# Kernel tuning notes

Measured on AMD Instinct MI355X. Metric: run time of the kernel, lower is better.

## Reference

```python
import jax, jax.numpy as jnp
import numpy as np

IOU_THRESHOLD = 0.5

def cxcywh_to_xyxy(b):
    cx, cy, w, h = jnp.split(b, 4, axis=-1)
    return jnp.concatenate([cx - 0.5 * w, cy - 0.5 * h, cx + 0.5 * w, cy + 0.5 * h], axis=-1)

def batched_giou(p_xyxy, t_xyxy):
    # p_xyxy: [B, N, 4], t_xyxy: [B, T, 4] -> giou: [B, N, T]
    p = p_xyxy[:, :, None, :]  # [B, N, 1, 4]
    t = t_xyxy[:, None, :, :]  # [B, 1, T, 4]
    area_p = (p_xyxy[..., 2] - p_xyxy[..., 0]) * (p_xyxy[..., 3] - p_xyxy[..., 1])  # [B, N]
    area_t = (t_xyxy[..., 2] - t_xyxy[..., 0]) * (t_xyxy[..., 3] - t_xyxy[..., 1])  # [B, T]
    lt = jnp.maximum(p[..., :2], t[..., :2])
    rb = jnp.minimum(p[..., 2:], t[..., 2:])
    wh = jnp.clip(rb - lt, 0.0)
    inter = wh[..., 0] * wh[..., 1]  # [B, N, T]
    union = area_p[:, :, None] + area_t[:, None, :] - inter
    iou = inter / union
    # enclosing box
    lt_e = jnp.minimum(p[..., :2], t[..., :2])
    rb_e = jnp.maximum(p[..., 2:], t[..., 2:])
    wh_e = jnp.clip(rb_e - lt_e, 0.0)
    area_e = wh_e[..., 0] * wh_e[..., 1]
    return iou - (area_e - union) / area_e

def setup_inputs() -> dict:
    key = jax.random.key(0)
    k1, k2 = jax.random.split(key)
    B, N, T = 128, 900, 300
    pred_boxes = jax.random.uniform(k1, (B, N, 4), dtype=jnp.float32)
    target_boxes = jax.random.uniform(k2, (B, T, 4), dtype=jnp.float32)
    target_mask = jnp.ones((B, T), dtype=bool)
    return {"pred_boxes": pred_boxes, "target_boxes": target_boxes, "target_mask": target_mask}

def reference(pred_boxes, target_boxes, target_mask):
    # pred_boxes: [B, N, 4] cxcywh; target_boxes: [B, T, 4] cxcywh (padded)
    p_xyxy = cxcywh_to_xyxy(pred_boxes)
    t_xyxy = cxcywh_to_xyxy(target_boxes)
    giou = batched_giou(p_xyxy, t_xyxy)  # [B, N, T]
    max_iou = jnp.max(giou, axis=1)      # [B, T] best GIoU per target
    pred_idx = jnp.argmax(giou, axis=1)  # [B, T] matched query per target
    valid = target_mask & (max_iou >= IOU_THRESHOLD)  # [B, T] match kept
    return pred_idx, valid, max_iou
```

## Files before the change

kernel.cpp:

```cpp
#include <hip/hip_runtime.h>


#define BB 128
#define NN 900
#define TT 300
#define NSPLIT 9
#define NPB 100
#define NPW 25
#define TPL 5
#define ALANES 60
#define MARGIN 2e-5f

__device__ __forceinline__ float giou_exact(float4 pb, float4 tb) {
#pragma clang fp contract(off)
    float px0 = pb.x - 0.5f * pb.z, py0 = pb.y - 0.5f * pb.w;
    float px1 = pb.x + 0.5f * pb.z, py1 = pb.y + 0.5f * pb.w;
    float tx0 = tb.x - 0.5f * tb.z, ty0 = tb.y - 0.5f * tb.w;
    float tx1 = tb.x + 0.5f * tb.z, ty1 = tb.y + 0.5f * tb.w;
    float pa = (px1 - px0) * (py1 - py0);
    float ta = (tx1 - tx0) * (ty1 - ty0);
    float w  = fmaxf(fminf(px1, tx1) - fmaxf(px0, tx0), 0.f);
    float h  = fmaxf(fminf(py1, ty1) - fmaxf(py0, ty0), 0.f);
    float inter = w * h;
    float uni   = pa + ta - inter;
    float iou   = inter / uni;
    float ew = fmaxf(fmaxf(px1, tx1) - fminf(px0, tx0), 0.f);
    float eh = fmaxf(fmaxf(py1, ty1) - fminf(py0, ty0), 0.f);
    float ea = ew * eh;
    return iou - (ea - uni) / ea;
}

__global__ __launch_bounds__(256, 6) void matcher_scan_kernel(
    const float* __restrict__ pred,
    const float* __restrict__ tgt,
    float* __restrict__ pbest,
    float* __restrict__ psec,
    int*   __restrict__ pidx)
{
    __shared__ float4 sp[NPB];
    __shared__ float  spa[NPB];
    __shared__ float  sbv[4 * TT], ssv[4 * TT];
    __shared__ int    siv[4 * TT];

    const int ns  = blockIdx.x % NSPLIT;
    const int b   = blockIdx.x / NSPLIT;
    const int tid = threadIdx.x;
    const int l   = tid & 63;
    const int ng  = tid >> 6;

    if (tid < NPB) {
        const float4 pb = ((const float4*)pred)[b * NN + ns * NPB + tid];
        float4 q;
        q.x = pb.x - 0.5f * pb.z;
        q.y = pb.y - 0.5f * pb.w;
        q.z = pb.x + 0.5f * pb.z;
        q.w = pb.y + 0.5f * pb.w;
        sp[tid]  = q;
        spa[tid] = (q.z - q.x) * (q.w - q.y);
    }

    float tx0[TPL], ty0[TPL], tx1[TPL], ty1[TPL], ta[TPL];
    #pragma unroll
    for (int j = 0; j < TPL; ++j) {
        tx0[j] = ty0[j] = tx1[j] = ty1[j] = ta[j] = 0.f;
        if (l < ALANES) {
            const float4 tb = ((const float4*)tgt)[b * TT + j * ALANES + l];
            tx0[j] = tb.x - 0.5f * tb.z;
            ty0[j] = tb.y - 0.5f * tb.w;
            tx1[j] = tb.x + 0.5f * tb.z;
            ty1[j] = tb.y + 0.5f * tb.w;
            ta[j]  = (tx1[j] - tx0[j]) * (ty1[j] - ty0[j]);
        }
    }
    __syncthreads();

    float best[TPL], sec[TPL];
    int   bl[TPL];
    #pragma unroll
    for (int j = 0; j < TPL; ++j) { best[j] = -INFINITY; sec[j] = -INFINITY; bl[j] = 0; }

    const int k0 = ng * NPW;
    for (int k = 0; k < NPW; ++k) {
        const float4 p = sp[k0 + k];
        const float pa = spa[k0 + k];
        #pragma unroll
        for (int j = 0; j < TPL; ++j) {
            const float w   = fmaxf(fminf(p.z, tx1[j]) - fmaxf(p.x, tx0[j]), 0.f);
            const float h   = fmaxf(fminf(p.w, ty1[j]) - fmaxf(p.y, ty0[j]), 0.f);
            const float inter = w * h;
            const float uni   = pa + ta[j] - inter;
            const float ew  = fmaxf(p.z, tx1[j]) - fminf(p.x, tx0[j]);
            const float eh  = fmaxf(p.w, ty1[j]) - fminf(p.y, ty0[j]);
            const float ea  = ew * eh;
            const float den = uni * ea;
            const float num = fmaf(inter, ea, fmaf(uni, uni, -den));
            const float g   = num * __builtin_amdgcn_rcpf(den);

            sec[j] = __builtin_amdgcn_fmed3f(g, best[j], sec[j]);
            if (g > best[j]) bl[j] = k;
            best[j] = fmaxf(best[j], g);
        }
    }

    if (l < ALANES) {
        #pragma unroll
        for (int j = 0; j < TPL; ++j) {
            const int u = j * ALANES + l;
            sbv[ng * TT + u] = best[j];
            ssv[ng * TT + u] = sec[j];
            siv[ng * TT + u] = k0 + bl[j];
        }
    }
    __syncthreads();

    for (int u = tid; u < TT; u += 256) {
        float bb = -INFINITY, ss = -INFINITY;
        int   bi = 0;
        #pragma unroll
        for (int s = 0; s < 4; ++s) {
            const float ob = sbv[s * TT + u];
            const float os = ssv[s * TT + u];
            const int   oi = siv[s * TT + u];
            ss = fmaxf(fminf(bb, ob), fmaxf(ss, os));
            if (ob > bb) { bb = ob; bi = oi; }
        }
        const int bt = b * TT + u;
        pbest[ns * BB * TT + bt] = bb;
        psec [ns * BB * TT + bt] = ss;
        pidx [ns * BB * TT + bt] = ns * NPB + bi;
    }
}

__global__ __launch_bounds__(256) void matcher_finish_kernel(
    const float* __restrict__ pbest,
    const float* __restrict__ psec,
    const int*   __restrict__ pidx,
    const float* __restrict__ pred,
    const float* __restrict__ tgt,
    const unsigned char* __restrict__ mask,
    float* __restrict__ out)
{
    __shared__ int sflag[256];
    __shared__ int scount;

    const int tid = threadIdx.x;
    const int bt  = blockIdx.x * 256 + tid;
    if (tid == 0) scount = 0;
    __syncthreads();

    float best = -INFINITY, second = -INFINITY;
    int   bidx = 0;
    #pragma unroll
    for (int s = 0; s < NSPLIT; ++s) {
        const float ob = pbest[s * BB * TT + bt];
        const float os = psec [s * BB * TT + bt];
        const int   oi = pidx [s * BB * TT + bt];
        second = fmaxf(fminf(best, ob), fmaxf(second, os));
        if (ob > best) { best = ob; bidx = oi; }
    }

    if (best - second > MARGIN) {
        const int b = bt / TT;
        const float4 pb = ((const float4*)pred)[b * NN + bidx];
        const float4 tb = ((const float4*)tgt)[bt];
        const float g = giou_exact(pb, tb);
        const bool valid = (mask[bt] != 0) && (g >= 0.5f);
        out[bt]               = (float)bidx;
        out[BB * TT + bt]     = valid ? 1.f : 0.f;
        out[2 * BB * TT + bt] = g;
    } else {
        const int pos = atomicAdd(&scount, 1);
        sflag[pos] = tid;
    }
    __syncthreads();

    const int cnt  = scount;
    const int lane = tid & 63;
    const int ng   = tid >> 6;
    for (int f = ng; f < cnt; f += 4) {
        const int fbt = blockIdx.x * 256 + sflag[f];
        const int b   = fbt / TT;
        const float4 tb = ((const float4*)tgt)[fbt];

        float bestx = -INFINITY;
        int   bix   = NN;
        for (int n = lane; n < NN; n += 64) {
            const float4 pb = ((const float4*)pred)[b * NN + n];
            const float g = giou_exact(pb, tb);
            if (g > bestx) { bestx = g; bix = n; }
        }
        for (int off = 32; off >= 1; off >>= 1) {
            const float ob = __shfl_xor(bestx, off);
            const int   oi = __shfl_xor(bix, off);
            if (ob > bestx || (ob == bestx && oi < bix)) { bestx = ob; bix = oi; }
        }
        if (lane == 0) {
            const bool valid = (mask[fbt] != 0) && (bestx >= 0.5f);
            out[fbt]               = (float)bix;
            out[BB * TT + fbt]     = valid ? 1.f : 0.f;
            out[2 * BB * TT + fbt] = bestx;
        }
    }
}

extern "C" void kernel_launch(void* const* d_in, const int* in_sizes, int n_in,
                              void* d_out, int out_size, void* d_ws, size_t ws_size,
                              hipStream_t stream) {
    const float* pred = (const float*)d_in[0];
    const float* tgt  = (const float*)d_in[1];
    const unsigned char* mask = (const unsigned char*)d_in[2];
    float* out = (float*)d_out;

    const size_t seg = (size_t)NSPLIT * BB * TT * 4;
    char* ws = (char*)d_ws;
    float* pbest = (float*)ws;
    float* psec  = (float*)(ws + seg);
    int*   pidx  = (int*)  (ws + 2 * seg);

    matcher_scan_kernel<<<dim3(BB * NSPLIT), dim3(256), 0, stream>>>(
        pred, tgt, pbest, psec, pidx);
    matcher_finish_kernel<<<dim3(BB * TT / 256), dim3(256), 0, stream>>>(
        pbest, psec, pidx, pred, tgt, mask, out);
}
```

Measured before the change: 98.54 us.

## Fuse scan and finish kernels via last-block-done atomic counter per batch

Merges the two-kernel scan/finish pipeline into one kernel. Each batch's last-finishing split block, found through a per-batch atomic counter and threadfences, performs the final reduction, exact GIoU recompute and fallback rescan. The pred tile is no longer staged in shared memory: each wave reads its pred boxes from global memory through a wave-uniform base and converts them inline. This removes one kernel launch and a pass over the workspace, but adds a memset launch, tail serialization on the last block, and extra conversion work inside the inner loop.

```diff
diff --git a/kernel.cpp b/kernel.cpp
--- a/kernel.cpp
+++ b/kernel.cpp
@@ -30,34 +30,27 @@
     return iou - (ea - uni) / ea;
 }
 
-__global__ __launch_bounds__(256, 6) void matcher_scan_kernel(
+__global__ __launch_bounds__(256) void matcher_kernel(
     const float* __restrict__ pred,
     const float* __restrict__ tgt,
+    const unsigned char* __restrict__ mask,
     float* __restrict__ pbest,
     float* __restrict__ psec,
-    int*   __restrict__ pidx)
+    int*   __restrict__ pidx,
+    unsigned int* __restrict__ done,
+    float* __restrict__ out)
 {
-    __shared__ float4 sp[NPB];
-    __shared__ float  spa[NPB];
-    __shared__ float  sbv[4 * TT], ssv[4 * TT];
-    __shared__ int    siv[4 * TT];
+    __shared__ float sbv[4 * TT], ssv[4 * TT];
+    __shared__ int   siv[4 * TT];
+    __shared__ int   slast;
+    __shared__ int   sflag[TT + 4];
+    __shared__ int   scount;
 
     const int ns  = blockIdx.x % NSPLIT;
     const int b   = blockIdx.x / NSPLIT;
     const int tid = threadIdx.x;
     const int l   = tid & 63;
     const int ng  = tid >> 6;
-
-    if (tid < NPB) {
-        const float4 pb = ((const float4*)pred)[b * NN + ns * NPB + tid];
-        float4 q;
-        q.x = pb.x - 0.5f * pb.z;
-        q.y = pb.y - 0.5f * pb.w;
-        q.z = pb.x + 0.5f * pb.z;
-        q.w = pb.y + 0.5f * pb.w;
-        sp[tid]  = q;
-        spa[tid] = (q.z - q.x) * (q.w - q.y);
-    }
 
     float tx0[TPL], ty0[TPL], tx1[TPL], ty1[TPL], ta[TPL];
     #pragma unroll
@@ -72,25 +65,28 @@
             ta[j]  = (tx1[j] - tx0[j]) * (ty1[j] - ty0[j]);
         }
     }
-    __syncthreads();
 
     float best[TPL], sec[TPL];
     int   bl[TPL];
     #pragma unroll
     for (int j = 0; j < TPL; ++j) { best[j] = -INFINITY; sec[j] = -INFINITY; bl[j] = 0; }
 
-    const int k0 = ng * NPW;
+    const int base = __builtin_amdgcn_readfirstlane(b * NN + ns * NPB + ng * NPW);
     for (int k = 0; k < NPW; ++k) {
-        const float4 p = sp[k0 + k];
-        const float pa = spa[k0 + k];
+        const float4 p = ((const float4*)pred)[base + k];
+        const float px0 = p.x - 0.5f * p.z;
+        const float py0 = p.y - 0.5f * p.w;
+        const float px1 = p.x + 0.5f * p.z;
+        const float py1 = p.y + 0.5f * p.w;
+        const float pa  = (px1 - px0) * (py1 - py0);
         #pragma unroll
         for (int j = 0; j < TPL; ++j) {
-            const float w   = fmaxf(fminf(p.z, tx1[j]) - fmaxf(p.x, tx0[j]), 0.f);
-            const float h   = fmaxf(fminf(p.w, ty1[j]) - fmaxf(p.y, ty0[j]), 0.f);
+            const float w   = fmaxf(fminf(px1, tx1[j]) - fmaxf(px0, tx0[j]), 0.f);
+            const float h   = fmaxf(fminf(py1, ty1[j]) - fmaxf(py0, ty0[j]), 0.f);
             const float inter = w * h;
             const float uni   = pa + ta[j] - inter;
-            const float ew  = fmaxf(p.z, tx1[j]) - fminf(p.x, tx0[j]);
-            const float eh  = fmaxf(p.w, ty1[j]) - fminf(p.y, ty0[j]);
+            const float ew  = fmaxf(px1, tx1[j]) - fminf(px0, tx0[j]);
+            const float eh  = fmaxf(py1, ty1[j]) - fminf(py0, ty0[j]);
             const float ea  = ew * eh;
             const float den = uni * ea;
             const float num = fmaf(inter, ea, fmaf(uni, uni, -den));
@@ -108,7 +104,7 @@
             const int u = j * ALANES + l;
             sbv[ng * TT + u] = best[j];
             ssv[ng * TT + u] = sec[j];
-            siv[ng * TT + u] = k0 + bl[j];
+            siv[ng * TT + u] = ng * NPW + bl[j];
         }
     }
     __syncthreads();
@@ -129,62 +125,53 @@
         psec [ns * BB * TT + bt] = ss;
         pidx [ns * BB * TT + bt] = ns * NPB + bi;
     }
-}
-
-__global__ __launch_bounds__(256) void matcher_finish_kernel(
-    const float* __restrict__ pbest,
-    const float* __restrict__ psec,
-    const int*   __restrict__ pidx,
-    const float* __restrict__ pred,
-    const float* __restrict__ tgt,
-    const unsigned char* __restrict__ mask,
-    float* __restrict__ out)
-{
-    __shared__ int sflag[256];
-    __shared__ int scount;
-
-    const int tid = threadIdx.x;
-    const int bt  = blockIdx.x * 256 + tid;
-    if (tid == 0) scount = 0;
+
+    __threadfence();
+    if (tid == 0) {
+        const unsigned int old = atomicAdd(&done[b], 1u);
+        slast = (old == NSPLIT - 1) ? 1 : 0;
+        scount = 0;
+    }
     __syncthreads();
-
-    float best = -INFINITY, second = -INFINITY;
-    int   bidx = 0;
-    #pragma unroll
-    for (int s = 0; s < NSPLIT; ++s) {
-        const float ob = pbest[s * BB * TT + bt];
-        const float os = psec [s * BB * TT + bt];
-        const int   oi = pidx [s * BB * TT + bt];
-        second = fmaxf(fminf(best, ob), fmaxf(second, os));
-        if (ob > best) { best = ob; bidx = oi; }
-    }
-
-    if (best - second > MARGIN) {
-        const int b = bt / TT;
-        const float4 pb = ((const float4*)pred)[b * NN + bidx];
-        const float4 tb = ((const float4*)tgt)[bt];
-        const float g = giou_exact(pb, tb);
-        const bool valid = (mask[bt] != 0) && (g >= 0.5f);
-        out[bt]               = (float)bidx;
-        out[BB * TT + bt]     = valid ? 1.f : 0.f;
-        out[2 * BB * TT + bt] = g;
-    } else {
-        const int pos = atomicAdd(&scount, 1);
-        sflag[pos] = tid;
+    if (!slast) return;
+    __threadfence();
+
+    for (int u = tid; u < TT; u += 256) {
+        float bb = -INFINITY, ss = -INFINITY;
+        int   bi = 0;
+        #pragma unroll
+        for (int s = 0; s < NSPLIT; ++s) {
+            const float ob = pbest[s * BB * TT + b * TT + u];
+            const float os = psec [s * BB * TT + b * TT + u];
+            const int   oi = pidx [s * BB * TT + b * TT + u];
+            ss = fmaxf(fminf(bb, ob), fmaxf(ss, os));
+            if (ob > bb) { bb = ob; bi = oi; }
+        }
+        const int bt = b * TT + u;
+        if (bb - ss > MARGIN) {
+            const float4 pb = ((const float4*)pred)[b * NN + bi];
+            const float4 tb = ((const float4*)tgt)[bt];
+            const float g = giou_exact(pb, tb);
+            const bool valid = (mask[bt] != 0) && (g >= 0.5f);
+            out[bt]               = (float)bi;
+            out[BB * TT + bt]     = valid ? 1.f : 0.f;
+            out[2 * BB * TT + bt] = g;
+        } else {
+            const int pos = atomicAdd(&scount, 1);
+            sflag[pos] = u;
+        }
     }
     __syncthreads();
 
-    const int cnt  = scount;
-    const int lane = tid & 63;
-    const int ng   = tid >> 6;
+    const int cnt = scount;
     for (int f = ng; f < cnt; f += 4) {
-        const int fbt = blockIdx.x * 256 + sflag[f];
-        const int b   = fbt / TT;
+        const int u   = sflag[f];
+        const int fbt = b * TT + u;
         const float4 tb = ((const float4*)tgt)[fbt];
 
         float bestx = -INFINITY;
         int   bix   = NN;
-        for (int n = lane; n < NN; n += 64) {
+        for (int n = l; n < NN; n += 64) {
             const float4 pb = ((const float4*)pred)[b * NN + n];
             const float g = giou_exact(pb, tb);
             if (g > bestx) { bestx = g; bix = n; }
@@ -194,7 +181,7 @@
             const int   oi = __shfl_xor(bix, off);
             if (ob > bestx || (ob == bestx && oi < bix)) { bestx = ob; bix = oi; }
         }
-        if (lane == 0) {
+        if (l == 0) {
             const bool valid = (mask[fbt] != 0) && (bestx >= 0.5f);
             out[fbt]               = (float)bix;
             out[BB * TT + fbt]     = valid ? 1.f : 0.f;
@@ -216,9 +203,9 @@
     float* pbest = (float*)ws;
     float* psec  = (float*)(ws + seg);
     int*   pidx  = (int*)  (ws + 2 * seg);
-
-    matcher_scan_kernel<<<dim3(BB * NSPLIT), dim3(256), 0, stream>>>(
-        pred, tgt, pbest, psec, pidx);
-    matcher_finish_kernel<<<dim3(BB * TT / 256), dim3(256), 0, stream>>>(
-        pbest, psec, pidx, pred, tgt, mask, out);
+    unsigned int* done = (unsigned int*)(ws + 3 * seg);
+
+    hipMemsetAsync(done, 0, BB * sizeof(unsigned int), stream);
+    matcher_kernel<<<dim3(BB * NSPLIT), dim3(256), 0, stream>>>(
+        pred, tgt, mask, pbest, psec, pidx, done, out);
 }
```

New measurement: 220.4 us. +123.7%, slower.
